# Kernel optimization log

Measured on AMD Instinct MI355X. Metric: run time of the kernel, lower is better.

The kernel has to match this reference:

```python
import jax, jax.numpy as jnp
import numpy as np

N = 100000      # nodes
E = 1600000     # edges (before self loops)
F_IN = 128      # num_graph_features
H = 2           # heads
C = 64          # out channels per head (output // 2)
G = 64          # graphs in batch
NEG_SLOPE = 0.2


def setup_inputs() -> dict:
    key = jax.random.key(0)
    ks = jax.random.split(key, 11)
    s = 0.1  # weight scale to keep activations well-conditioned
    return {
        "x": jax.random.normal(ks[0], (N, F_IN), jnp.float32),
        "edge_index": jax.random.randint(ks[1], (2, E), 0, N, jnp.int32),
        "batch": jnp.sort(jax.random.randint(ks[2], (N,), 0, G, jnp.int32)),
        "W1": jax.random.normal(ks[3], (F_IN, H * C), jnp.float32) * s,
        "a1_src": jax.random.normal(ks[4], (H, C), jnp.float32) * s,
        "a1_dst": jax.random.normal(ks[5], (H, C), jnp.float32) * s,
        "b1": jnp.zeros((H * C,), jnp.float32),
        "W2": jax.random.normal(ks[6], (H * C, H * C), jnp.float32) * s,
        "a2_src": jax.random.normal(ks[7], (H, C), jnp.float32) * s,
        "a2_dst": jax.random.normal(ks[8], (H, C), jnp.float32) * s,
        "b2": jnp.zeros((H * C,), jnp.float32),
    }


def gat_conv(x, src, dst, W, a_src, a_dst, bias, n):
    # PyG GATConv (shared lin, concat=True): h: [n, H, C]
    h = (x @ W).reshape(n, H, C)
    alpha_src = jnp.sum(h * a_src, axis=-1)          # [n, H]
    alpha_dst = jnp.sum(h * a_dst, axis=-1)          # [n, H]
    e = jax.nn.leaky_relu(alpha_src[src] + alpha_dst[dst], NEG_SLOPE)  # [E', H]
    # segment softmax over edges grouped by destination node
    m = jax.ops.segment_max(e, dst, num_segments=n)  # [n, H]
    ex = jnp.exp(e - m[dst])
    denom = jax.ops.segment_sum(ex, dst, num_segments=n)
    alpha = ex / (denom[dst] + 1e-16)                # [E', H]
    out = jax.ops.segment_sum(alpha[:, :, None] * h[src], dst, num_segments=n)
    return out.reshape(n, H * C) + bias


def reference(x, edge_index, batch, W1, a1_src, a1_dst, b1, W2, a2_src, a2_dst, b2):
    # edge/node masks assumed all-valid (identity filtering)
    loops = jnp.arange(N, dtype=edge_index.dtype)    # add_self_loops=True
    src = jnp.concatenate([edge_index[0], loops])
    dst = jnp.concatenate([edge_index[1], loops])
    h1 = jax.nn.relu(gat_conv(x, src, dst, W1, a1_src, a1_dst, b1, N))
    h2 = gat_conv(h1, src, dst, W2, a2_src, a2_dst, b2, N)
    # global_mean_pool over batch ids
    pooled = jax.ops.segment_sum(h2, batch, num_segments=G)
    counts = jax.ops.segment_sum(jnp.ones((N,), h2.dtype), batch, num_segments=G)
    return pooled / jnp.maximum(counts, 1.0)[:, None]
```

## Files before the change

kernel.cpp:

```cpp
#include <hip/hip_runtime.h>

#define N_NODES 100000
#define N_EDGES 1600000
#define F_IN    128
#define HC      128
#define NGRAPH  64
#define NEG_SLOPE 0.2f

static constexpr int TOT_E = N_EDGES + N_NODES;

#define CHUNK  2048
#define NBLK   831
#define NBUCK  196

#define GEMM_B 1563
#define CNT_B  391

typedef __bf16 bf16x8 __attribute__((ext_vector_type(8)));
typedef float  f32x4  __attribute__((ext_vector_type(4)));
typedef float  f32x2  __attribute__((ext_vector_type(2)));

__device__ __forceinline__ unsigned short f2bf_rne(float f) {
    unsigned u = __float_as_uint(f);
    u += 0x7fffu + ((u >> 16) & 1u);
    return (unsigned short)(u >> 16);
}
__device__ __forceinline__ float bf2f(unsigned b) {
    return __uint_as_float(b << 16);
}
__device__ __forceinline__ unsigned char f2fp8(float f) {
    return (unsigned char)(__builtin_amdgcn_cvt_pk_fp8_f32(f, f, 0, 0) & 0xff);
}


__device__ __forceinline__ void binpart_body(int blk, int t,
                                             const int* __restrict__ ei,
                                             unsigned* __restrict__ pairs,
                                             int* __restrict__ seg_start,
                                             int* __restrict__ seg_cnt,
                                             int* cnt, int* wtot) {
    int lane = t & 63, w = t >> 6;
    long base = (long)blk * CHUNK;

    cnt[t] = 0;
    __syncthreads();

    for (int j = t; j < CHUNK; j += 256) {
        long i = base + j;
        int d = -1;
        if (i < N_EDGES)    d = ei[N_EDGES + i];
        else if (i < TOT_E) d = (int)(i - N_EDGES);
        if (d >= 0) atomicAdd(&cnt[d >> 9], 1);
    }
    __syncthreads();

    int c = cnt[t];
    int x = c;
#pragma unroll
    for (int off = 1; off < 64; off <<= 1) {
        int v = __shfl_up(x, off);
        if (lane >= off) x += v;
    }
    if (lane == 63) wtot[w] = x;
    __syncthreads();
    int add = 0;
#pragma unroll
    for (int k = 0; k < 3; ++k) if (k < w) add += wtot[k];
    x += add;
    int st = x - c;
    if (t < NBUCK) {
        seg_start[(size_t)blk * NBUCK + t] = st;
        seg_cnt[(size_t)blk * NBUCK + t]   = c;
    }
    __syncthreads();
    cnt[t] = st;
    __syncthreads();

    for (int j = t; j < CHUNK; j += 256) {
        long i = base + j;
        int s = -1, d = -1;
        if (i < N_EDGES)    { s = ei[i]; d = ei[N_EDGES + i]; }
        else if (i < TOT_E) { s = (int)(i - N_EDGES); d = s; }
        if (d >= 0) {
            int pos = atomicAdd(&cnt[d >> 9], 1);
            pairs[base + pos] = ((unsigned)s << 9) | ((unsigned)d & 511u);
        }
    }
}

template<bool BF16IN>
__device__ __forceinline__ void gemm_body(int gbid, int t,
                                          const void* __restrict__ Xv,
                                          const unsigned short* __restrict__ Wt,
                                          unsigned char* __restrict__ Hout,
                                          const float* __restrict__ a_src,
                                          const float* __restrict__ a_dst,
                                          float* __restrict__ asrc,
                                          float* __restrict__ adst,
                                          unsigned short* A_lds) {
    int lane = t & 63, wave = t >> 6;
    int wc = wave & 1, wr = wave >> 1;
    int base = gbid * 64;

    bf16x8 Bf[4][4];
    {
        int colb = wc * 64 + (lane & 15);
        int kbb  = lane >> 4;
#pragma unroll
        for (int ct = 0; ct < 4; ++ct)
#pragma unroll
            for (int ks = 0; ks < 4; ++ks) {
                int kb = kbb + 4 * ks;
                Bf[ct][ks] = *(const bf16x8*)&Wt[(size_t)kb * (HC * 8) + (colb + ct * 16) * 8];
            }
    }

#pragma unroll
    for (int it = 0; it < 8; ++it) {
        int i = t + it * 256;
        int row = i >> 5, c4 = i & 31, k0 = c4 * 4;
        uint2 pk; pk.x = 0; pk.y = 0;
        if (base + row < N_NODES) {
            if (BF16IN) {
                pk = ((const uint2*)Xv)[(size_t)(base + row) * 32 + c4];
            } else {
                float4 v = ((const float4*)Xv)[(size_t)(base + row) * 32 + c4];
                pk.x = (unsigned)f2bf_rne(v.x) | ((unsigned)f2bf_rne(v.y) << 16);
                pk.y = (unsigned)f2bf_rne(v.z) | ((unsigned)f2bf_rne(v.w) << 16);
            }
        }
        int byte = row * 256 + (((k0 >> 3) ^ (row & 7)) << 4) + (k0 & 4) * 2;
        *(uint2*)((char*)A_lds + byte) = pk;
    }
    __syncthreads();

    f32x4 acc[2][4] = {};
#pragma unroll
    for (int ks = 0; ks < 4; ++ks) {
        bf16x8 Af[2];
#pragma unroll
        for (int r = 0; r < 2; ++r) {
            int row = wr * 32 + r * 16 + (lane & 15);
            int kb  = ks * 4 + (lane >> 4);
            int byte = row * 256 + ((kb ^ (row & 7)) << 4);
            Af[r] = *(const bf16x8*)((const char*)A_lds + byte);
        }
#pragma unroll
        for (int ct = 0; ct < 4; ++ct) {
            acc[0][ct] = __builtin_amdgcn_mfma_f32_16x16x32_bf16(Af[0], Bf[ct][ks], acc[0][ct], 0, 0, 0);
            acc[1][ct] = __builtin_amdgcn_mfma_f32_16x16x32_bf16(Af[1], Bf[ct][ks], acc[1][ct], 0, 0, 0);
        }
    }

#pragma unroll
    for (int r = 0; r < 2; ++r) {
        int row0 = base + wr * 32 + r * 16 + (lane >> 4) * 4;
#pragma unroll
        for (int reg = 0; reg < 4; ++reg) {
            int row = row0 + reg;
            if (row < N_NODES) {
#pragma unroll
                for (int ct = 0; ct < 4; ++ct) {
                    int col = wc * 64 + ct * 16 + (lane & 15);
                    Hout[(size_t)row * HC + col] = f2fp8(acc[r][ct][reg]);
                }
            }
        }
    }

    float as_c[4], ad_c[4];
#pragma unroll
    for (int ct = 0; ct < 4; ++ct) {
        int ch = wc * 64 + ct * 16 + (lane & 15);
        as_c[ct] = a_src[ch];
        ad_c[ct] = a_dst[ch];
    }
#pragma unroll
    for (int r = 0; r < 2; ++r) {
#pragma unroll
        for (int reg = 0; reg < 4; ++reg) {
            float ps = acc[r][0][reg] * as_c[0] + acc[r][1][reg] * as_c[1]
                     + acc[r][2][reg] * as_c[2] + acc[r][3][reg] * as_c[3];
            float pd = acc[r][0][reg] * ad_c[0] + acc[r][1][reg] * ad_c[1]
                     + acc[r][2][reg] * ad_c[2] + acc[r][3][reg] * ad_c[3];
#pragma unroll
            for (int off = 1; off < 16; off <<= 1) {
                ps += __shfl_xor(ps, off);
                pd += __shfl_xor(pd, off);
            }
            if ((lane & 15) == 0) {
                int row = base + wr * 32 + r * 16 + (lane >> 4) * 4 + reg;
                if (row < N_NODES) {
                    asrc[(size_t)row * 2 + wc] = ps;
                    adst[(size_t)row * 2 + wc] = pd;
                }
            }
        }
    }
}


__global__ __launch_bounds__(256) void fused_main(const float* __restrict__ x,
                                                  const unsigned short* __restrict__ wt1,
                                                  unsigned char* __restrict__ hA,
                                                  const float* __restrict__ a1s,
                                                  const float* __restrict__ a1d,
                                                  float* __restrict__ asrc,
                                                  float* __restrict__ adst,
                                                  const int* __restrict__ ei,
                                                  unsigned* __restrict__ pairs,
                                                  int* __restrict__ seg_start,
                                                  int* __restrict__ seg_cnt,
                                                  const int* __restrict__ batch,
                                                  int* __restrict__ counts) {
    __shared__ unsigned short A_lds[64 * F_IN];
    __shared__ int cnt[256];
    __shared__ int wtot[4];
    __shared__ int loc[NGRAPH];
    int bid = blockIdx.x, t = threadIdx.x;

    if (bid < 2 * NBLK) {
        if (bid & 1) binpart_body(bid >> 1, t, ei, pairs, seg_start, seg_cnt, cnt, wtot);
        else         gemm_body<false>(bid >> 1, t, x, wt1, hA, a1s, a1d, asrc, adst, A_lds);
    } else if (bid < NBLK + GEMM_B) {
        gemm_body<false>(bid - NBLK, t, x, wt1, hA, a1s, a1d, asrc, adst, A_lds);
    } else {
        int cb = bid - (NBLK + GEMM_B);
        if (t < NGRAPH) loc[t] = 0;
        __syncthreads();
        int i = cb * 256 + t;
        if (i < N_NODES) atomicAdd(&loc[batch[i]], 1);
        __syncthreads();
        if (t < NGRAPH && loc[t]) atomicAdd(&counts[t], loc[t]);
    }
}


__global__ __launch_bounds__(256) void gemm2_kernel(const unsigned short* __restrict__ Xv,
                                                    const unsigned short* __restrict__ Wt,
                                                    unsigned char* __restrict__ Hout,
                                                    const float* __restrict__ a_src,
                                                    const float* __restrict__ a_dst,
                                                    float* __restrict__ asrc,
                                                    float* __restrict__ adst) {
    __shared__ unsigned short A_lds[64 * F_IN];
    gemm_body<true>(blockIdx.x, threadIdx.x, Xv, Wt, Hout, a_src, a_dst, asrc, adst, A_lds);
}


__global__ __launch_bounds__(256) void btot_kernel(const int* __restrict__ seg_cnt, int* __restrict__ btot) {
    int b = blockIdx.x, t = threadIdx.x;
    int s = 0;
    for (int j = t; j < NBLK; j += 256) s += seg_cnt[(size_t)j * NBUCK + b];
    for (int off = 32; off; off >>= 1) s += __shfl_down(s, off);
    __shared__ int ws[4];
    int lane = t & 63, w = t >> 6;
    if (lane == 0) ws[w] = s;
    __syncthreads();
    if (t == 0) btot[b] = ws[0] + ws[1] + ws[2] + ws[3];
}

__global__ __launch_bounds__(256) void bbase_kernel(const int* __restrict__ btot, int* __restrict__ bbase) {
    int t = threadIdx.x;
    int lane = t & 63, w = t >> 6;
    int v = (t < NBUCK) ? btot[t] : 0;
    int x = v;
#pragma unroll
    for (int off = 1; off < 64; off <<= 1) {
        int u = __shfl_up(x, off);
        if (lane >= off) x += u;
    }
    __shared__ int wt[4];
    if (lane == 63) wt[w] = x;
    __syncthreads();
    int add = 0;
#pragma unroll
    for (int k = 0; k < 3; ++k) if (k < w) add += wt[k];
    x += add;
    if (t < NBUCK) bbase[t] = x - v;
}


__global__ __launch_bounds__(1024) void bucket_build(const unsigned* __restrict__ pairs,
                                                     const int* __restrict__ seg_start,
                                                     const int* __restrict__ seg_cnt,
                                                     const int* __restrict__ bbase,
                                                     int* __restrict__ offs,
                                                     int* __restrict__ csr_src) {
    int b = blockIdx.x, t = threadIdx.x;
    int nodeBase = b << 9;
    __shared__ int cur[512];
    __shared__ int pref[NBLK];
    __shared__ int sstart[NBLK];
    __shared__ int wt2[16];

    if (t < 512) cur[t] = 0;
    for (int j = t; j < NBLK; j += 1024) {
        pref[j]   = seg_cnt[(size_t)j * NBUCK + b];
        sstart[j] = seg_start[(size_t)j * NBUCK + b];
    }
    __syncthreads();
    for (int off = 1; off < NBLK; off <<= 1) {
        int v = 0;
        if (t < NBLK && t >= off) v = pref[t - off];
        __syncthreads();
        if (t < NBLK) pref[t] += v;
        __syncthreads();
    }
    int M = pref[NBLK - 1];

    for (int j = t; j < M; j += 1024) {
        int lo = 0, hi = NBLK - 1;
        while (lo < hi) { int mid = (lo + hi) >> 1; if (pref[mid] > j) hi = mid; else lo = mid + 1; }
        int within = j - (lo ? pref[lo - 1] : 0);
        unsigned wd = pairs[(size_t)lo * CHUNK + sstart[lo] + within];
        atomicAdd(&cur[wd & 511u], 1);
    }
    __syncthreads();

    int lane = t & 63, w = t >> 6;
    int myc = (t < 512) ? cur[t] : 0;
    int x = myc;
#pragma unroll
    for (int off = 1; off < 64; off <<= 1) {
        int u = __shfl_up(x, off);
        if (lane >= off) x += u;
    }
    if (lane == 63) wt2[w] = x;
    __syncthreads();
    int add = 0;
#pragma unroll
    for (int k = 0; k < 15; ++k) if (k < w) add += wt2[k];
    x += add;
    int gstart = bbase[b] + x - myc;
    if (t < 512) {
        if (nodeBase + t <= N_NODES) offs[nodeBase + t] = gstart;
        cur[t] = gstart;
    }
    __syncthreads();

    for (int j = t; j < M; j += 1024) {
        int lo = 0, hi = NBLK - 1;
        while (lo < hi) { int mid = (lo + hi) >> 1; if (pref[mid] > j) hi = mid; else lo = mid + 1; }
        int within = j - (lo ? pref[lo - 1] : 0);
        unsigned wd = pairs[(size_t)lo * CHUNK + sstart[lo] + within];
        int pos = atomicAdd(&cur[wd & 511u], 1);
        csr_src[pos] = (int)(wd >> 9);
    }
}


__global__ __launch_bounds__(256) void wtconv_both(const float* __restrict__ W1, const float* __restrict__ W2,
                                                   unsigned short* __restrict__ Wt1, unsigned short* __restrict__ Wt2) {
    int i = blockIdx.x * 256 + threadIdx.x;
    const float* W = (i < F_IN * HC) ? W1 : W2;
    unsigned short* Wt = (i < F_IN * HC) ? Wt1 : Wt2;
    int j = (i < F_IN * HC) ? i : i - F_IN * HC;
    if (j < F_IN * HC) {
        int k = j >> 7, col = j & 127;
        Wt[(size_t)(k >> 3) * (HC * 8) + col * 8 + (k & 7)] = f2bf_rne(W[j]);
    }
}


__global__ __launch_bounds__(256) void agg_kernel(const int* __restrict__ offs, const int* __restrict__ csr_src,
                                                  const float* __restrict__ asrc, const float* __restrict__ adst,
                                                  const unsigned char* __restrict__ Hin,
                                                  const float* __restrict__ bias,
                                                  unsigned short* __restrict__ Hout, int do_relu) {
    int wid  = (blockIdx.x * 256 + threadIdx.x) >> 6;
    int lane = threadIdx.x & 63;
    if (wid >= N_NODES) return;
    int beg = offs[wid], end = offs[wid + 1];
    int grp   = lane >> 3;
    int head  = grp & 1;
    int eslot = grp >> 1;
    int q8    = lane & 7;
    float2 adv = *(const float2*)&adst[(size_t)wid * 2];
    float madst = head ? adv.y : adv.x;
    const float2* av = (const float2*)asrc;
    const unsigned char* hbase = Hin + head * 64 + q8 * 8;

    float den = 0.f;
    float a0c = 0.f, a1c = 0.f, a2c = 0.f, a3c = 0.f;
    float a4c = 0.f, a5c = 0.f, a6c = 0.f, a7c = 0.f;

    for (int e = beg + eslot; e < end; e += 8) {
        int en = e + 4;
        bool v1 = en < end;
        int s0 = csr_src[e];
        int s1 = v1 ? csr_src[en] : s0;
        float2 aa0 = av[s0];
        float2 aa1 = av[s1];
        uint2 g0 = *(const uint2*)&hbase[(size_t)s0 * HC];
        uint2 g1 = *(const uint2*)&hbase[(size_t)s1 * HC];
        float l0 = (head ? aa0.y : aa0.x) + madst; l0 = l0 > 0.f ? l0 : NEG_SLOPE * l0;
        float l1 = (head ? aa1.y : aa1.x) + madst; l1 = l1 > 0.f ? l1 : NEG_SLOPE * l1;
        float w0 = __expf(l0);
        float w1 = v1 ? __expf(l1) : 0.f;
        den += w0 + w1;
        f32x2 p00 = __builtin_amdgcn_cvt_pk_f32_fp8(g0.x, 0);
        f32x2 p01 = __builtin_amdgcn_cvt_pk_f32_fp8(g0.x, 1);
        f32x2 p02 = __builtin_amdgcn_cvt_pk_f32_fp8(g0.y, 0);
        f32x2 p03 = __builtin_amdgcn_cvt_pk_f32_fp8(g0.y, 1);
        f32x2 p10 = __builtin_amdgcn_cvt_pk_f32_fp8(g1.x, 0);
        f32x2 p11 = __builtin_amdgcn_cvt_pk_f32_fp8(g1.x, 1);
        f32x2 p12 = __builtin_amdgcn_cvt_pk_f32_fp8(g1.y, 0);
        f32x2 p13 = __builtin_amdgcn_cvt_pk_f32_fp8(g1.y, 1);
        a0c = fmaf(w1, p10.x, fmaf(w0, p00.x, a0c));
        a1c = fmaf(w1, p10.y, fmaf(w0, p00.y, a1c));
        a2c = fmaf(w1, p11.x, fmaf(w0, p01.x, a2c));
        a3c = fmaf(w1, p11.y, fmaf(w0, p01.y, a3c));
        a4c = fmaf(w1, p12.x, fmaf(w0, p02.x, a4c));
        a5c = fmaf(w1, p12.y, fmaf(w0, p02.y, a5c));
        a6c = fmaf(w1, p13.x, fmaf(w0, p03.x, a6c));
        a7c = fmaf(w1, p13.y, fmaf(w0, p03.y, a7c));
    }

#pragma unroll
    for (int off = 16; off <= 32; off <<= 1) {
        den += __shfl_xor(den, off);
        a0c += __shfl_xor(a0c, off);
        a1c += __shfl_xor(a1c, off);
        a2c += __shfl_xor(a2c, off);
        a3c += __shfl_xor(a3c, off);
        a4c += __shfl_xor(a4c, off);
        a5c += __shfl_xor(a5c, off);
        a6c += __shfl_xor(a6c, off);
        a7c += __shfl_xor(a7c, off);
    }

    if (lane < 16) {
        float inv = 1.0f / den;
        float4 b0 = *(const float4*)&bias[lane * 8];
        float4 b1 = *(const float4*)&bias[lane * 8 + 4];
        float o0 = fmaf(a0c, inv, b0.x);
        float o1 = fmaf(a1c, inv, b0.y);
        float o2 = fmaf(a2c, inv, b0.z);
        float o3 = fmaf(a3c, inv, b0.w);
        float o4 = fmaf(a4c, inv, b1.x);
        float o5 = fmaf(a5c, inv, b1.y);
        float o6 = fmaf(a6c, inv, b1.z);
        float o7 = fmaf(a7c, inv, b1.w);
        if (do_relu) {
            o0 = fmaxf(o0, 0.f); o1 = fmaxf(o1, 0.f); o2 = fmaxf(o2, 0.f); o3 = fmaxf(o3, 0.f);
            o4 = fmaxf(o4, 0.f); o5 = fmaxf(o5, 0.f); o6 = fmaxf(o6, 0.f); o7 = fmaxf(o7, 0.f);
        }
        uint4 st;
        st.x = (unsigned)f2bf_rne(o0) | ((unsigned)f2bf_rne(o1) << 16);
        st.y = (unsigned)f2bf_rne(o2) | ((unsigned)f2bf_rne(o3) << 16);
        st.z = (unsigned)f2bf_rne(o4) | ((unsigned)f2bf_rne(o5) << 16);
        st.w = (unsigned)f2bf_rne(o6) | ((unsigned)f2bf_rne(o7) << 16);
        *(uint4*)&Hout[(size_t)wid * HC + lane * 8] = st;
    }
}


__global__ __launch_bounds__(256) void pool_kernel(const unsigned short* __restrict__ H2,
                                                   const int* __restrict__ counts,
                                                   float* __restrict__ out) {
    int g = blockIdx.x;
    int chunk = blockIdx.y;
    __shared__ int soff, scnt;
    if (threadIdx.x == 0) {
        int s = 0;
        for (int i = 0; i < g; ++i) s += counts[i];
        soff = s; scnt = counts[g];
    }
    __syncthreads();
    int start = soff, cnt = scnt;
    int r = threadIdx.x >> 7;
    int c = threadIdx.x & 127;
    float acc = 0.f;
    for (int v = chunk * 2 + r; v < cnt; v += 16)
        acc += bf2f((unsigned)H2[(size_t)(start + v) * HC + c]);
    float inv = 1.0f / fmaxf((float)cnt, 1.0f);
    atomicAdd(&out[g * HC + c], acc * inv);
}


extern "C" void kernel_launch(void* const* d_in, const int* in_sizes, int n_in,
                              void* d_out, int out_size, void* d_ws, size_t ws_size,
                              hipStream_t stream) {
    const float* x     = (const float*)d_in[0];
    const int*   ei    = (const int*)d_in[1];
    const int*   batch = (const int*)d_in[2];
    const float* W1    = (const float*)d_in[3];
    const float* a1s   = (const float*)d_in[4];
    const float* a1d   = (const float*)d_in[5];
    const float* b1    = (const float*)d_in[6];
    const float* W2    = (const float*)d_in[7];
    const float* a2s   = (const float*)d_in[8];
    const float* a2d   = (const float*)d_in[9];
    const float* b2    = (const float*)d_in[10];
    float* out = (float*)d_out;

    char* ws = (char*)d_ws;
    const size_t NH = (size_t)N_NODES * HC;
    unsigned char* hA = (unsigned char*)ws;
    unsigned short* hB = (unsigned short*)(ws + NH);
    unsigned* pairs = (unsigned*)(hB + NH);
    float* asrc = (float*)(pairs + (size_t)NBLK * CHUNK);
    float* adst = asrc + (size_t)N_NODES * 2;
    unsigned short* wt1 = (unsigned short*)(adst + (size_t)N_NODES * 2);
    unsigned short* wt2 = wt1 + F_IN * HC;
    int*   offs = (int*)(wt2 + F_IN * HC);
    int*   csr  = offs + (N_NODES + 1);
    int*   seg_start = csr + TOT_E;
    int*   seg_cnt   = seg_start + (size_t)NBLK * NBUCK;
    int*   btot = seg_cnt + (size_t)NBLK * NBUCK;
    int*   bbase = btot + NBUCK;
    int*   counts = bbase + NBUCK;

    hipMemsetAsync(counts, 0, NGRAPH * sizeof(int), stream);
    hipMemsetAsync(out, 0, (size_t)out_size * sizeof(float), stream);

    wtconv_both<<<(2 * F_IN * HC + 255) / 256, 256, 0, stream>>>(W1, W2, wt1, wt2);

    fused_main<<<GEMM_B + NBLK + CNT_B, 256, 0, stream>>>(x, wt1, hA, a1s, a1d, asrc, adst,
                                                          ei, pairs, seg_start, seg_cnt,
                                                          batch, counts);

    btot_kernel<<<NBUCK, 256, 0, stream>>>(seg_cnt, btot);
    bbase_kernel<<<1, 256, 0, stream>>>(btot, bbase);
    bucket_build<<<NBUCK, 1024, 0, stream>>>(pairs, seg_start, seg_cnt, bbase, offs, csr);

    int waveBlocks = (N_NODES + 3) / 4;

    agg_kernel<<<waveBlocks, 256, 0, stream>>>(offs, csr, asrc, adst, hA, b1, hB, 1);

    gemm2_kernel<<<GEMM_B, 256, 0, stream>>>(hB, wt2, hA, a2s, a2d, asrc, adst);
    agg_kernel<<<waveBlocks, 256, 0, stream>>>(offs, csr, asrc, adst, hA, b2, hB, 0);

    pool_kernel<<<dim3(NGRAPH, 8), 256, 0, stream>>>(hB, counts, out);
}
```

Baseline: 254.8 us.

## Pack bf16 source attention scores into CSR entries to avoid per-edge gathers

The CSR array now stores a uint2 per edge: the source index plus both heads' alpha_src packed as bf16. The CSR build fills these for layer 1, and a new aug_kernel refreshes them after gemm2 for layer 2. This removes the dependent random gather of asrc inside the aggregation loop. The cost is an extra pass over all edges, doubled CSR bandwidth, and bf16 rounding of attention logits. The aggregation lane mapping is also reorganised (16 lanes per edge slot covering both heads) and the accumulators use packed f32x2 math.

```diff
diff --git a/kernel.cpp b/kernel.cpp
--- a/kernel.cpp
+++ b/kernel.cpp
@@ -285,8 +285,9 @@
                                                      const int* __restrict__ seg_start,
                                                      const int* __restrict__ seg_cnt,
                                                      const int* __restrict__ bbase,
+                                                     const float* __restrict__ asrc,
                                                      int* __restrict__ offs,
-                                                     int* __restrict__ csr_src) {
+                                                     uint2* __restrict__ csr2) {
     int b = blockIdx.x, t = threadIdx.x;
     int nodeBase = b << 9;
     __shared__ int cur[512];
@@ -345,8 +346,20 @@
         int within = j - (lo ? pref[lo - 1] : 0);
         unsigned wd = pairs[(size_t)lo * CHUNK + sstart[lo] + within];
         int pos = atomicAdd(&cur[wd & 511u], 1);
-        csr_src[pos] = (int)(wd >> 9);
-    }
+        unsigned s = wd >> 9;
+        float2 av = *(const float2*)&asrc[(size_t)s * 2];
+        unsigned ap = (unsigned)f2bf_rne(av.x) | ((unsigned)f2bf_rne(av.y) << 16);
+        csr2[pos] = make_uint2(s, ap);
+    }
+}
+
+
+__global__ __launch_bounds__(256) void aug_kernel(uint2* __restrict__ csr2, const float* __restrict__ asrc) {
+    int e = blockIdx.x * 256 + threadIdx.x;
+    if (e >= TOT_E) return;
+    unsigned s = csr2[e].x;
+    float2 av = *(const float2*)&asrc[(size_t)s * 2];
+    csr2[e].y = (unsigned)f2bf_rne(av.x) | ((unsigned)f2bf_rne(av.y) << 16);
 }
 
 
@@ -363,8 +376,8 @@
 }
 
 
-__global__ __launch_bounds__(256) void agg_kernel(const int* __restrict__ offs, const int* __restrict__ csr_src,
-                                                  const float* __restrict__ asrc, const float* __restrict__ adst,
+__global__ __launch_bounds__(256) void agg_kernel(const int* __restrict__ offs, const uint2* __restrict__ csr2,
+                                                  const float* __restrict__ adst,
                                                   const unsigned char* __restrict__ Hin,
                                                   const float* __restrict__ bias,
                                                   unsigned short* __restrict__ Hout, int do_relu) {
@@ -372,51 +385,42 @@
     int lane = threadIdx.x & 63;
     if (wid >= N_NODES) return;
     int beg = offs[wid], end = offs[wid + 1];
-    int grp   = lane >> 3;
-    int head  = grp & 1;
-    int eslot = grp >> 1;
-    int q8    = lane & 7;
-    float2 adv = *(const float2*)&adst[(size_t)wid * 2];
-    float madst = head ? adv.y : adv.x;
-    const float2* av = (const float2*)asrc;
-    const unsigned char* hbase = Hin + head * 64 + q8 * 8;
+    int grp  = lane >> 4;
+    int q    = lane & 15;
+    int head = q >> 3;
+    float madst = adst[(size_t)wid * 2 + head];
+    const unsigned char* hbase = Hin + q * 8;
 
     float den = 0.f;
-    float a0c = 0.f, a1c = 0.f, a2c = 0.f, a3c = 0.f;
-    float a4c = 0.f, a5c = 0.f, a6c = 0.f, a7c = 0.f;
-
-    for (int e = beg + eslot; e < end; e += 8) {
+    f32x2 ac01 = {0.f, 0.f}, ac23 = {0.f, 0.f}, ac45 = {0.f, 0.f}, ac67 = {0.f, 0.f};
+
+    for (int e = beg + grp; e < end; e += 8) {
         int en = e + 4;
         bool v1 = en < end;
-        int s0 = csr_src[e];
-        int s1 = v1 ? csr_src[en] : s0;
-        float2 aa0 = av[s0];
-        float2 aa1 = av[s1];
-        uint2 g0 = *(const uint2*)&hbase[(size_t)s0 * HC];
-        uint2 g1 = *(const uint2*)&hbase[(size_t)s1 * HC];
-        float l0 = (head ? aa0.y : aa0.x) + madst; l0 = l0 > 0.f ? l0 : NEG_SLOPE * l0;
-        float l1 = (head ? aa1.y : aa1.x) + madst; l1 = l1 > 0.f ? l1 : NEG_SLOPE * l1;
+        uint2 c0 = csr2[e];
+        uint2 c1 = v1 ? csr2[en] : c0;
+        float aa0 = bf2f(head ? (c0.y >> 16) : (c0.y & 0xffffu));
+        float aa1 = bf2f(head ? (c1.y >> 16) : (c1.y & 0xffffu));
+        uint2 g0 = *(const uint2*)&hbase[(size_t)c0.x * HC];
+        uint2 g1 = *(const uint2*)&hbase[(size_t)c1.x * HC];
+        float l0 = aa0 + madst; l0 = l0 > 0.f ? l0 : NEG_SLOPE * l0;
+        float l1 = aa1 + madst; l1 = l1 > 0.f ? l1 : NEG_SLOPE * l1;
         float w0 = __expf(l0);
         float w1 = v1 ? __expf(l1) : 0.f;
         den += w0 + w1;
-        f32x2 p00 = __builtin_amdgcn_cvt_pk_f32_fp8(g0.x, 0);
-        f32x2 p01 = __builtin_amdgcn_cvt_pk_f32_fp8(g0.x, 1);
-        f32x2 p02 = __builtin_amdgcn_cvt_pk_f32_fp8(g0.y, 0);
-        f32x2 p03 = __builtin_amdgcn_cvt_pk_f32_fp8(g0.y, 1);
-        f32x2 p10 = __builtin_amdgcn_cvt_pk_f32_fp8(g1.x, 0);
-        f32x2 p11 = __builtin_amdgcn_cvt_pk_f32_fp8(g1.x, 1);
-        f32x2 p12 = __builtin_amdgcn_cvt_pk_f32_fp8(g1.y, 0);
-        f32x2 p13 = __builtin_amdgcn_cvt_pk_f32_fp8(g1.y, 1);
-        a0c = fmaf(w1, p10.x, fmaf(w0, p00.x, a0c));
-        a1c = fmaf(w1, p10.y, fmaf(w0, p00.y, a1c));
-        a2c = fmaf(w1, p11.x, fmaf(w0, p01.x, a2c));
-        a3c = fmaf(w1, p11.y, fmaf(w0, p01.y, a3c));
-        a4c = fmaf(w1, p12.x, fmaf(w0, p02.x, a4c));
-        a5c = fmaf(w1, p12.y, fmaf(w0, p02.y, a5c));
-        a6c = fmaf(w1, p13.x, fmaf(w0, p03.x, a6c));
-        a7c = fmaf(w1, p13.y, fmaf(w0, p03.y, a7c));
-    }
-
+        f32x2 w0v = {w0, w0}, w1v = {w1, w1};
+        ac01 += __builtin_amdgcn_cvt_pk_f32_fp8(g0.x, 0) * w0v;
+        ac23 += __builtin_amdgcn_cvt_pk_f32_fp8(g0.x, 1) * w0v;
+        ac45 += __builtin_amdgcn_cvt_pk_f32_fp8(g0.y, 0) * w0v;
+        ac67 += __builtin_amdgcn_cvt_pk_f32_fp8(g0.y, 1) * w0v;
+        ac01 += __builtin_amdgcn_cvt_pk_f32_fp8(g1.x, 0) * w1v;
+        ac23 += __builtin_amdgcn_cvt_pk_f32_fp8(g1.x, 1) * w1v;
+        ac45 += __builtin_amdgcn_cvt_pk_f32_fp8(g1.y, 0) * w1v;
+        ac67 += __builtin_amdgcn_cvt_pk_f32_fp8(g1.y, 1) * w1v;
+    }
+
+    float a0c = ac01.x, a1c = ac01.y, a2c = ac23.x, a3c = ac23.y;
+    float a4c = ac45.x, a5c = ac45.y, a6c = ac67.x, a7c = ac67.y;
 #pragma unroll
     for (int off = 16; off <= 32; off <<= 1) {
         den += __shfl_xor(den, off);
@@ -432,8 +436,8 @@
 
     if (lane < 16) {
         float inv = 1.0f / den;
-        float4 b0 = *(const float4*)&bias[lane * 8];
-        float4 b1 = *(const float4*)&bias[lane * 8 + 4];
+        float4 b0 = *(const float4*)&bias[q * 8];
+        float4 b1 = *(const float4*)&bias[q * 8 + 4];
         float o0 = fmaf(a0c, inv, b0.x);
         float o1 = fmaf(a1c, inv, b0.y);
         float o2 = fmaf(a2c, inv, b0.z);
@@ -451,7 +455,7 @@
         st.y = (unsigned)f2bf_rne(o2) | ((unsigned)f2bf_rne(o3) << 16);
         st.z = (unsigned)f2bf_rne(o4) | ((unsigned)f2bf_rne(o5) << 16);
         st.w = (unsigned)f2bf_rne(o6) | ((unsigned)f2bf_rne(o7) << 16);
-        *(uint4*)&Hout[(size_t)wid * HC + lane * 8] = st;
+        *(uint4*)&Hout[(size_t)wid * HC + q * 8] = st;
     }
 }
 
@@ -505,8 +509,8 @@
     unsigned short* wt1 = (unsigned short*)(adst + (size_t)N_NODES * 2);
     unsigned short* wt2 = wt1 + F_IN * HC;
     int*   offs = (int*)(wt2 + F_IN * HC);
-    int*   csr  = offs + (N_NODES + 1);
-    int*   seg_start = csr + TOT_E;
+    uint2* csr2 = (uint2*)(offs + (N_NODES + 2));
+    int*   seg_start = (int*)(csr2 + TOT_E);
     int*   seg_cnt   = seg_start + (size_t)NBLK * NBUCK;
     int*   btot = seg_cnt + (size_t)NBLK * NBUCK;
     int*   bbase = btot + NBUCK;
@@ -523,14 +527,16 @@
 
     btot_kernel<<<NBUCK, 256, 0, stream>>>(seg_cnt, btot);
     bbase_kernel<<<1, 256, 0, stream>>>(btot, bbase);
-    bucket_build<<<NBUCK, 1024, 0, stream>>>(pairs, seg_start, seg_cnt, bbase, offs, csr);
+    bucket_build<<<NBUCK, 1024, 0, stream>>>(pairs, seg_start, seg_cnt, bbase, asrc, offs, csr2);
 
     int waveBlocks = (N_NODES + 3) / 4;
-
-    agg_kernel<<<waveBlocks, 256, 0, stream>>>(offs, csr, asrc, adst, hA, b1, hB, 1);
+    int augBlocks  = (TOT_E + 255) / 256;
+
+    agg_kernel<<<waveBlocks, 256, 0, stream>>>(offs, csr2, adst, hA, b1, hB, 1);
 
     gemm2_kernel<<<GEMM_B, 256, 0, stream>>>(hB, wt2, hA, a2s, a2d, asrc, adst);
-    agg_kernel<<<waveBlocks, 256, 0, stream>>>(offs, csr, asrc, adst, hA, b2, hB, 0);
+    aug_kernel<<<augBlocks, 256, 0, stream>>>(csr2, asrc);
+    agg_kernel<<<waveBlocks, 256, 0, stream>>>(offs, csr2, adst, hA, b2, hB, 0);
 
     pool_kernel<<<dim3(NGRAPH, 8), 256, 0, stream>>>(hB, counts, out);
 }
```

Result: no change. 258.5 us (+1.4%).
